# Kernel optimization log

Measured on AMD Instinct MI355X. Metric: run time of the kernel, lower is better.

The kernel has to match this reference:

```python
import jax, jax.numpy as jnp
import numpy as np

N, E, IN, H, D = 50000, 800000, 256, 4, 32
NEG_SLOPE = 0.2


def setup_inputs() -> dict:
    key = jax.random.key(0)
    ks = jax.random.split(key, 11)
    feat = jax.random.normal(ks[0], (N, IN), jnp.float32)
    src = jax.random.randint(ks[1], (E,), 0, N, jnp.int32)
    dst = jax.random.randint(ks[2], (E,), 0, N, jnp.int32)
    # ppmi in [1, 10) so log(log(ppmi)) path is non-trivial
    ppmi = 1.0 + 9.0 * jax.random.uniform(ks[3], (E,), jnp.float32)
    eps_src = jax.random.normal(ks[4], (N, H, 1), jnp.float32)
    eps_dst = jax.random.normal(ks[5], (N, H, 1), jnp.float32)
    W = jax.random.normal(ks[6], (IN, H * D), jnp.float32) * (1.0 / np.sqrt(IN))
    mu_src = jax.random.normal(ks[7], (1, H, D), jnp.float32) * 0.02
    mu_dst = jax.random.normal(ks[8], (1, H, D), jnp.float32) * 0.02
    lam_src = jax.random.normal(ks[9], (1, H, D), jnp.float32) * 0.02
    lam_dst = jax.random.normal(ks[10], (1, H, D), jnp.float32) * 0.02
    return dict(feat=feat, src=src, dst=dst, ppmi=ppmi, eps_src=eps_src,
                eps_dst=eps_dst, W=W, mu_src=mu_src, mu_dst=mu_dst,
                lam_src=lam_src, lam_dst=lam_dst)


def reference(feat, src, dst, ppmi, eps_src, eps_dst, W, mu_src, mu_dst, lam_src, lam_dst):
    n = feat.shape[0]
    h, d = mu_src.shape[1], mu_src.shape[2]
    ft = (feat @ W).reshape(n, h, d)                      # [N,H,D]
    # per-node attention scalars (src == dst node set here)
    mu_s = (ft * mu_src).sum(-1, keepdims=True)           # [N,H,1]
    lam_s = (ft * lam_src).sum(-1, keepdims=True)
    mu_d = (ft * mu_dst).sum(-1, keepdims=True)
    lam_d = (ft * lam_src).sum(-1, keepdims=True)         # original uses lam_src here (replicated)
    # reparameterize z = eps * exp(0.5*logvar) + mu
    z_src = eps_src * jnp.exp(0.5 * lam_s) + mu_s
    z_dst = eps_dst * jnp.exp(0.5 * lam_d) + mu_d
    e = jax.nn.leaky_relu(z_src[src] + z_dst[dst], NEG_SLOPE)   # [E,H,1]
    scale = jnp.clip(jnp.log(jnp.clip(jnp.log(ppmi), 1.0, None)), 1.0, None)
    e2 = e * scale[:, None, None]
    # edge softmax over destination segments
    emax = jax.ops.segment_max(e2, dst, num_segments=n)   # [N,H,1]
    ee = jnp.exp(e2 - emax[dst])
    denom = jax.ops.segment_sum(ee, dst, num_segments=n)
    a = ee / denom[dst]                                    # [E,H,1]
    # weighted scatter-sum aggregation: u_mul_e + sum
    rst = jax.ops.segment_sum(ft[src] * a, dst, num_segments=n)  # [N,H,D]
    return rst, mu_s + mu_d, lam_s + lam_d
```

## Files before the change

kernel.cpp:

```cpp
#include <hip/hip_runtime.h>

#define N_NODES 50000
#define N_EDGES 800000
#define IN_DIM  256
#define NH      4
#define HD      128
#define NEG_SLOPE 0.2f
#define SCAN_BLOCKS ((N_NODES + 255) / 256)
#define HIST_BLOCKS ((N_EDGES + 255) / 256)
#define WT_BLOCKS   ((HD * IN_DIM) / 256)
#define K1B_BLOCKS  ((N_NODES * NH + 255) / 256)

typedef short          v8s __attribute__((ext_vector_type(8)));
typedef float          v4f __attribute__((ext_vector_type(4)));
typedef unsigned short us8 __attribute__((ext_vector_type(8)));
typedef int            v4i __attribute__((ext_vector_type(4)));

__device__ __forceinline__ unsigned short f2bf(float f)
{
    unsigned int u = __float_as_uint(f);
    u += 0x7fffu + ((u >> 16) & 1u);
    return (unsigned short)(u >> 16);
}
__device__ __forceinline__ float bf2f(unsigned int bits16)
{
    return __uint_as_float(bits16 << 16);
}

__device__ __forceinline__ float edge_scale(float p)
{
    const float lp = fmaxf(__logf(p), 1.0f);
    return fmaxf(__logf(lp), 1.0f);
}

__global__ __launch_bounds__(256) void k_wt_hist(
    const float* __restrict__ W, unsigned short* __restrict__ Wt_bf,
    const int* __restrict__ dst, int* __restrict__ counts,
    int* __restrict__ rank)
{
    const int b = blockIdx.x;
    if (b < HIST_BLOCKS) {
        const int e = b * 256 + threadIdx.x;
        if (e < N_EDGES) rank[e] = atomicAdd(&counts[dst[e]], 1);
    } else {
        const int idx = (b - HIST_BLOCKS) * 256 + threadIdx.x;
        const int n = idx >> 8;
        const int k = idx & 255;
        Wt_bf[n * IN_DIM + k] = f2bf(W[(size_t)k * HD + n]);
    }
}

#define AS 40
#define CS 136

__global__ __launch_bounds__(256) void k1_mfma(
    const float* __restrict__ feat, const unsigned short* __restrict__ Wt_bf,
    unsigned short* __restrict__ ft_bf)
{
    __shared__ ushort smem[17408];
    ushort* A_sh = smem;
    ushort* B_sh = smem + 128 * AS;

    const int t    = threadIdx.x;
    const int lane = t & 63;
    const int wv   = t >> 6;
    const int r0   = blockIdx.x * 128;

    const int arow = t >> 3;
    const int akk  = (t & 7) * 4;
    int rA[4];
#pragma unroll
    for (int p = 0; p < 4; ++p) rA[p] = min(r0 + arow + 32 * p, N_NODES - 1);
    const int bn  = t >> 2;
    const int bk8 = (t & 3) * 8;

    float4 fa[4];
    us8    fb[2];

#define LOADC(kc0)                                                              \
    do {                                                                        \
        _Pragma("unroll")                                                       \
        for (int p = 0; p < 4; ++p)                                             \
            fa[p] = *(const float4*)(feat + (size_t)rA[p] * IN_DIM + (kc0) + akk); \
        _Pragma("unroll")                                                       \
        for (int p = 0; p < 2; ++p)                                             \
            fb[p] = *(const us8*)(Wt_bf + (size_t)(bn + 64 * p) * IN_DIM + (kc0) + bk8); \
    } while (0)

    v4f acc[2][8];
#pragma unroll
    for (int i = 0; i < 2; ++i)
#pragma unroll
        for (int j = 0; j < 8; ++j) acc[i][j] = (v4f)(0.0f);

    const int frow = lane & 15;
    const int fq   = lane >> 4;

    LOADC(0);

    for (int c = 0; c < IN_DIM / 32; ++c) {
        __syncthreads();
#pragma unroll
        for (int p = 0; p < 4; ++p) {
            ushort4 u;
            u.x = f2bf(fa[p].x); u.y = f2bf(fa[p].y);
            u.z = f2bf(fa[p].z); u.w = f2bf(fa[p].w);
            *(ushort4*)(A_sh + (arow + 32 * p) * AS + akk) = u;
        }
#pragma unroll
        for (int p = 0; p < 2; ++p)
            *(us8*)(B_sh + (bn + 64 * p) * AS + bk8) = fb[p];
        __syncthreads();

        if (c + 1 < IN_DIM / 32) LOADC((c + 1) * 32);

        v8s a0 = *(const v8s*)(A_sh + (wv * 32 + frow) * AS + fq * 8);
        v8s a1 = *(const v8s*)(A_sh + (wv * 32 + 16 + frow) * AS + fq * 8);
        v8s bfr[8];
#pragma unroll
        for (int nf = 0; nf < 8; ++nf)
            bfr[nf] = *(const v8s*)(B_sh + (nf * 16 + frow) * AS + fq * 8);
#pragma unroll
        for (int nf = 0; nf < 8; ++nf) {
            acc[0][nf] = __builtin_amdgcn_mfma_f32_16x16x32_bf16(
                a0, bfr[nf], acc[0][nf], 0, 0, 0);
            acc[1][nf] = __builtin_amdgcn_mfma_f32_16x16x32_bf16(
                a1, bfr[nf], acc[1][nf], 0, 0, 0);
        }
    }

    __syncthreads();
    ushort* Cw = smem + wv * (32 * CS);
#pragma unroll
    for (int mf = 0; mf < 2; ++mf)
#pragma unroll
        for (int nf = 0; nf < 8; ++nf)
#pragma unroll
            for (int r = 0; r < 4; ++r)
                Cw[(mf * 16 + fq * 4 + r) * CS + nf * 16 + frow] =
                    f2bf(acc[mf][nf][r]);
    __syncthreads();

#pragma unroll
    for (int p = 0; p < 8; ++p) {
        const int row_l = (lane >> 4) + 4 * p;
        const int colv  = (lane & 15) * 8;
        const us8 val = *(const us8*)(Cw + row_l * CS + colv);
        const int grow = r0 + wv * 32 + row_l;
        if (grow < N_NODES)
            *(us8*)(ft_bf + (size_t)grow * HD + colv) = val;
    }
}

__global__ __launch_bounds__(256) void k_k1b_scanlocal(
    const int* __restrict__ counts, int* __restrict__ local,
    int* __restrict__ bsums,
    const unsigned short* __restrict__ ft_bf,
    const float* __restrict__ mu_src, const float* __restrict__ mu_dst,
    const float* __restrict__ lam_src,
    const float* __restrict__ eps_src, const float* __restrict__ eps_dst,
    float* __restrict__ z_src_ws, float* __restrict__ z_dst_ws,
    float* __restrict__ mu_out, float* __restrict__ lam_out)
{
    __shared__ int sh[256];
    const int b = blockIdx.x;
    const int t = threadIdx.x;

    if (b < SCAN_BLOCKS) {
        const int i = b * 256 + t;
        const int v = (i < N_NODES) ? counts[i] : 0;
        sh[t] = v;
        __syncthreads();
#pragma unroll
        for (int off = 1; off < 256; off <<= 1) {
            int x = (t >= off) ? sh[t - off] : 0;
            __syncthreads();
            sh[t] += x;
            __syncthreads();
        }
        if (i < N_NODES) local[i] = sh[t] - v;
        if (t == 255) bsums[b] = sh[255];
        return;
    }

    const int g = (b - SCAN_BLOCKS) * 256 + t;
    if (g >= N_NODES * NH) return;
    const int row = g >> 2;
    const int h   = g & 3;

    const unsigned short* fr = ft_bf + (size_t)row * HD + h * 32;
    const float* ms = mu_src + h * 32;
    const float* md = mu_dst + h * 32;
    const float* ls = lam_src + h * 32;

    float pm = 0.0f, pd = 0.0f, pl = 0.0f;
#pragma unroll
    for (int v = 0; v < 4; ++v) {
        const us8 u = *(const us8*)(fr + v * 8);
#pragma unroll
        for (int j = 0; j < 8; ++j) {
            const float f = bf2f(u[j]);
            const int   i = v * 8 + j;
            pm = fmaf(f, ms[i], pm);
            pd = fmaf(f, md[i], pd);
            pl = fmaf(f, ls[i], pl);
        }
    }
    const float sdev = expf(0.5f * pl);
    z_src_ws[g] = eps_src[g] * sdev + pm;
    z_dst_ws[g] = eps_dst[g] * sdev + pd;
    mu_out[g]   = pm + pd;
    lam_out[g]  = 2.0f * pl;
}

__global__ __launch_bounds__(256) void k_scan_bsums(
    const int* __restrict__ bsums, int* __restrict__ bscan)
{
    __shared__ int sh[256];
    const int t = threadIdx.x;
    const int v = (t < SCAN_BLOCKS) ? bsums[t] : 0;
    sh[t] = v;
    __syncthreads();
#pragma unroll
    for (int off = 1; off < 256; off <<= 1) {
        int x = (t >= off) ? sh[t - off] : 0;
        __syncthreads();
        sh[t] += x;
        __syncthreads();
    }
    if (t < SCAN_BLOCKS) bscan[t] = sh[t] - v;
}

__global__ __launch_bounds__(256) void k_scan_add(
    const int* __restrict__ local, const int* __restrict__ bscan,
    int* __restrict__ offsets)
{
    const int i = blockIdx.x * 256 + threadIdx.x;
    if (i >= N_NODES) return;
    offsets[i] = local[i] + bscan[blockIdx.x];
}

__global__ __launch_bounds__(256) void k_scatter(
    const int* __restrict__ src, const int* __restrict__ dst,
    const float* __restrict__ ppmi, const int* __restrict__ rank,
    const int* __restrict__ offsets, v4i* __restrict__ rec_sorted)
{
    const int e = blockIdx.x * 256 + threadIdx.x;
    if (e >= N_EDGES) return;
    const int d0 = dst[e];
    const int j  = offsets[d0] + rank[e];
    v4i rec;
    rec.x = src[e];
    rec.y = __float_as_int(edge_scale(ppmi[e]));
    rec.z = 0;
    rec.w = 0;
    __builtin_nontemporal_store(rec, rec_sorted + j);
}

__device__ __forceinline__ float edge_w1(float zs, float zd, float sc)
{
    float v = zs + zd;
    v = (v >= 0.0f) ? v : NEG_SLOPE * v;
    return __expf(v * sc);
}

__global__ __launch_bounds__(64) void k3_csr(
    const int* __restrict__ offsets, const int* __restrict__ counts,
    const v4i* __restrict__ rec_sorted,
    const float* __restrict__ z_src_ws, const float* __restrict__ z_dst_ws,
    const unsigned int* __restrict__ ft_u32, float2* __restrict__ rst2)
{
    const int node = blockIdx.x;
    const int lane = threadIdx.x;
    const int h    = lane >> 4;
    const int start = offsets[node];
    const int deg   = counts[node];
    const float zd  = z_dst_ws[node * NH + h];

    float ax = 0.0f, ay = 0.0f, wsum = 0.0f;

    int i = 0;
    for (; i + 4 <= deg; i += 4) {
        const v4i r0 = __builtin_nontemporal_load(rec_sorted + start + i);
        const v4i r1 = __builtin_nontemporal_load(rec_sorted + start + i + 1);
        const v4i r2 = __builtin_nontemporal_load(rec_sorted + start + i + 2);
        const v4i r3 = __builtin_nontemporal_load(rec_sorted + start + i + 3);
        const float z0 = z_src_ws[r0.x * NH + h];
        const float z1 = z_src_ws[r1.x * NH + h];
        const float z2 = z_src_ws[r2.x * NH + h];
        const float z3 = z_src_ws[r3.x * NH + h];
        const unsigned f0 = ft_u32[(size_t)r0.x * (HD / 2) + lane];
        const unsigned f1 = ft_u32[(size_t)r1.x * (HD / 2) + lane];
        const unsigned f2 = ft_u32[(size_t)r2.x * (HD / 2) + lane];
        const unsigned f3 = ft_u32[(size_t)r3.x * (HD / 2) + lane];
        const float w0 = edge_w1(z0, zd, __int_as_float(r0.y));
        const float w1 = edge_w1(z1, zd, __int_as_float(r1.y));
        const float w2 = edge_w1(z2, zd, __int_as_float(r2.y));
        const float w3 = edge_w1(z3, zd, __int_as_float(r3.y));
        ax = fmaf(bf2f(f0 & 0xffffu), w0, ax);
        ay = fmaf(bf2f(f0 >> 16),     w0, ay);
        ax = fmaf(bf2f(f1 & 0xffffu), w1, ax);
        ay = fmaf(bf2f(f1 >> 16),     w1, ay);
        ax = fmaf(bf2f(f2 & 0xffffu), w2, ax);
        ay = fmaf(bf2f(f2 >> 16),     w2, ay);
        ax = fmaf(bf2f(f3 & 0xffffu), w3, ax);
        ay = fmaf(bf2f(f3 >> 16),     w3, ay);
        wsum += (w0 + w1) + (w2 + w3);
    }
    for (; i < deg; ++i) {
        const v4i r0 = __builtin_nontemporal_load(rec_sorted + start + i);
        const float z0 = z_src_ws[r0.x * NH + h];
        const unsigned f0 = ft_u32[(size_t)r0.x * (HD / 2) + lane];
        const float w0 = edge_w1(z0, zd, __int_as_float(r0.y));
        ax = fmaf(bf2f(f0 & 0xffffu), w0, ax);
        ay = fmaf(bf2f(f0 >> 16),     w0, ay);
        wsum += w0;
    }

    const float inv = (wsum > 0.0f) ? 1.0f / wsum : 0.0f;
    rst2[(size_t)node * (HD / 2) + lane] = make_float2(ax * inv, ay * inv);
}

extern "C" void kernel_launch(void* const* d_in, const int* in_sizes, int n_in,
                              void* d_out, int out_size, void* d_ws, size_t ws_size,
                              hipStream_t stream)
{
    const float* feat    = (const float*)d_in[0];
    const int*   src     = (const int*)  d_in[1];
    const int*   dst     = (const int*)  d_in[2];
    const float* ppmi    = (const float*)d_in[3];
    const float* eps_src = (const float*)d_in[4];
    const float* eps_dst = (const float*)d_in[5];
    const float* W       = (const float*)d_in[6];
    const float* mu_src  = (const float*)d_in[7];
    const float* mu_dst  = (const float*)d_in[8];
    const float* lam_src = (const float*)d_in[9];

    float* out     = (float*)d_out;
    float* rst     = out;
    float* mu_out  = out + (size_t)N_NODES * HD;
    float* lam_out = mu_out + (size_t)N_NODES * NH;

    char* wsb = (char*)d_ws;
    v4i*            rec_s  = (v4i*)wsb;
    unsigned short* ft_bf  = (unsigned short*)(wsb + (size_t)N_EDGES * 16);
    unsigned short* Wt_bf  = ft_bf + (size_t)N_NODES * HD;
    float*          zs_ws  = (float*)(Wt_bf + (size_t)HD * IN_DIM);
    float*          zd_ws  = zs_ws + (size_t)N_NODES * NH;
    int*            counts = (int*)(zd_ws + (size_t)N_NODES * NH);
    int*            local  = counts + N_NODES;
    int*            offsets= local + N_NODES;
    int*            bsums  = offsets + N_NODES;
    int*            bscan  = bsums + 256;
    int*            rank   = bscan + 256;

    hipMemsetAsync(counts, 0, N_NODES * sizeof(int), stream);

    k_wt_hist<<<HIST_BLOCKS + WT_BLOCKS, 256, 0, stream>>>(
        W, Wt_bf, dst, counts, rank);

    k1_mfma<<<(N_NODES + 127) / 128, 256, 0, stream>>>(feat, Wt_bf, ft_bf);

    k_k1b_scanlocal<<<SCAN_BLOCKS + K1B_BLOCKS, 256, 0, stream>>>(
        counts, local, bsums,
        ft_bf, mu_src, mu_dst, lam_src, eps_src, eps_dst,
        zs_ws, zd_ws, mu_out, lam_out);

    k_scan_bsums<<<1, 256, 0, stream>>>(bsums, bscan);
    k_scan_add<<<SCAN_BLOCKS, 256, 0, stream>>>(local, bscan, offsets);

    k_scatter<<<HIST_BLOCKS, 256, 0, stream>>>(
        src, dst, ppmi, rank, offsets, rec_s);

    k3_csr<<<N_NODES, 64, 0, stream>>>(
        offsets, counts, rec_s, zs_ws, zd_ws,
        (const unsigned int*)ft_bf, (float2*)rst);
}
```

Measured before the change: 240.1 us.

## Split each wavefront across four edges with 16-byte feature gathers in CSR aggregation

The aggregation kernel now gives each 16-lane group of a 64-lane wave its own edge, so four edges are gathered at once. Each lane loads a 128-bit chunk (8 bf16 values) of the source feature row instead of one 32-bit word. Partial sums are merged across the four groups with xor shuffles before the normalized write-out, and tail edges are masked to zero weight. This aims to issue fewer, wider gather instructions and expose more memory parallelism per wave. In exchange it adds shuffle reduction work and a dynamically indexed accumulator array, which could be lowered to selects or scratch memory.

```diff
diff --git a/kernel.cpp b/kernel.cpp
--- a/kernel.cpp
+++ b/kernel.cpp
@@ -268,57 +268,58 @@
     const int* __restrict__ offsets, const int* __restrict__ counts,
     const v4i* __restrict__ rec_sorted,
     const float* __restrict__ z_src_ws, const float* __restrict__ z_dst_ws,
-    const unsigned int* __restrict__ ft_u32, float2* __restrict__ rst2)
+    const uint4* __restrict__ ft_u128, float2* __restrict__ rst2)
 {
     const int node = blockIdx.x;
     const int lane = threadIdx.x;
-    const int h    = lane >> 4;
+    const int es   = lane >> 4;
+    const int li   = lane & 15;
+    const int h    = li >> 2;
     const int start = offsets[node];
     const int deg   = counts[node];
     const float zd  = z_dst_ws[node * NH + h];
 
-    float ax = 0.0f, ay = 0.0f, wsum = 0.0f;
+    float acc[8] = {0, 0, 0, 0, 0, 0, 0, 0};
+    float wsum = 0.0f;
+
+#define K3_EDGE(EI)                                                            \
+    do {                                                                       \
+        const int  ei  = (EI);                                                 \
+        const int  idx = start + ((ei < deg) ? ei : 0);                        \
+        const v4i  r   = __builtin_nontemporal_load(rec_sorted + idx);         \
+        const float zs = z_src_ws[r.x * NH + h];                               \
+        const uint4 f  = ft_u128[(size_t)r.x * 16 + li];                       \
+        float w = edge_w1(zs, zd, __int_as_float(r.y));                        \
+        if (ei >= deg) w = 0.0f;                                               \
+        acc[0] = fmaf(bf2f(f.x & 0xffffu), w, acc[0]);                         \
+        acc[1] = fmaf(bf2f(f.x >> 16),     w, acc[1]);                         \
+        acc[2] = fmaf(bf2f(f.y & 0xffffu), w, acc[2]);                         \
+        acc[3] = fmaf(bf2f(f.y >> 16),     w, acc[3]);                         \
+        acc[4] = fmaf(bf2f(f.z & 0xffffu), w, acc[4]);                         \
+        acc[5] = fmaf(bf2f(f.z >> 16),     w, acc[5]);                         \
+        acc[6] = fmaf(bf2f(f.w & 0xffffu), w, acc[6]);                         \
+        acc[7] = fmaf(bf2f(f.w >> 16),     w, acc[7]);                         \
+        wsum += w;                                                             \
+    } while (0)
 
     int i = 0;
-    for (; i + 4 <= deg; i += 4) {
-        const v4i r0 = __builtin_nontemporal_load(rec_sorted + start + i);
-        const v4i r1 = __builtin_nontemporal_load(rec_sorted + start + i + 1);
-        const v4i r2 = __builtin_nontemporal_load(rec_sorted + start + i + 2);
-        const v4i r3 = __builtin_nontemporal_load(rec_sorted + start + i + 3);
-        const float z0 = z_src_ws[r0.x * NH + h];
-        const float z1 = z_src_ws[r1.x * NH + h];
-        const float z2 = z_src_ws[r2.x * NH + h];
-        const float z3 = z_src_ws[r3.x * NH + h];
-        const unsigned f0 = ft_u32[(size_t)r0.x * (HD / 2) + lane];
-        const unsigned f1 = ft_u32[(size_t)r1.x * (HD / 2) + lane];
-        const unsigned f2 = ft_u32[(size_t)r2.x * (HD / 2) + lane];
-        const unsigned f3 = ft_u32[(size_t)r3.x * (HD / 2) + lane];
-        const float w0 = edge_w1(z0, zd, __int_as_float(r0.y));
-        const float w1 = edge_w1(z1, zd, __int_as_float(r1.y));
-        const float w2 = edge_w1(z2, zd, __int_as_float(r2.y));
-        const float w3 = edge_w1(z3, zd, __int_as_float(r3.y));
-        ax = fmaf(bf2f(f0 & 0xffffu), w0, ax);
-        ay = fmaf(bf2f(f0 >> 16),     w0, ay);
-        ax = fmaf(bf2f(f1 & 0xffffu), w1, ax);
-        ay = fmaf(bf2f(f1 >> 16),     w1, ay);
-        ax = fmaf(bf2f(f2 & 0xffffu), w2, ax);
-        ay = fmaf(bf2f(f2 >> 16),     w2, ay);
-        ax = fmaf(bf2f(f3 & 0xffffu), w3, ax);
-        ay = fmaf(bf2f(f3 >> 16),     w3, ay);
-        wsum += (w0 + w1) + (w2 + w3);
-    }
-    for (; i < deg; ++i) {
-        const v4i r0 = __builtin_nontemporal_load(rec_sorted + start + i);
-        const float z0 = z_src_ws[r0.x * NH + h];
-        const unsigned f0 = ft_u32[(size_t)r0.x * (HD / 2) + lane];
-        const float w0 = edge_w1(z0, zd, __int_as_float(r0.y));
-        ax = fmaf(bf2f(f0 & 0xffffu), w0, ax);
-        ay = fmaf(bf2f(f0 >> 16),     w0, ay);
-        wsum += w0;
+    for (; i + 8 <= deg; i += 8) {
+        K3_EDGE(i + es);
+        K3_EDGE(i + 4 + es);
+    }
+    if (i < deg) K3_EDGE(i + es);
+    if (i + 4 < deg) K3_EDGE(i + 4 + es);
+
+#pragma unroll
+    for (int m = 16; m <= 32; m <<= 1) {
+        wsum += __shfl_xor(wsum, m, 64);
+#pragma unroll
+        for (int j = 0; j < 8; ++j) acc[j] += __shfl_xor(acc[j], m, 64);
     }
 
     const float inv = (wsum > 0.0f) ? 1.0f / wsum : 0.0f;
-    rst2[(size_t)node * (HD / 2) + lane] = make_float2(ax * inv, ay * inv);
+    rst2[(size_t)node * 64 + li * 4 + es] =
+        make_float2(acc[es * 2] * inv, acc[es * 2 + 1] * inv);
 }
 
 extern "C" void kernel_launch(void* const* d_in, const int* in_sizes, int n_in,
@@ -374,5 +375,5 @@
 
     k3_csr<<<N_NODES, 64, 0, stream>>>(
         offsets, counts, rec_s, zs_ws, zd_ws,
-        (const unsigned int*)ft_bf, (float2*)rst);
-}
+        (const uint4*)ft_bf, (float2*)rst);
+}
```

Result: no change. 239.2 us (-0.3%).
